# Kernel optimization log

Measured on AMD Instinct MI355X. Metric: run time of the kernel, lower is better.

Reference implementation:

```python
import jax, jax.numpy as jnp
import numpy as np


def setup_inputs() -> dict:
    key = jax.random.key(0)
    k1, k2, k3, k4 = jax.random.split(key, 4)
    B, OUT, IN, K = 64, 4096, 25088, 32
    x = jax.random.normal(k1, (B, IN), dtype=jnp.float32)
    labels = jax.random.randint(k2, (OUT, IN), 0, K, dtype=jnp.int32)
    centroids = jax.random.normal(k3, (K,), dtype=jnp.float32)
    bias = jax.random.normal(k4, (OUT,), dtype=jnp.float32)
    return {"x": x, "labels": labels, "centroids": centroids, "bias": bias}


def reference(x, labels, centroids, bias):
    # Dequantize: reconstruct weight [OUT, IN] by looking labels up in the codebook
    W = centroids[labels]                      # [OUT, IN] gather
    # addmm(bias, x, W.T): [B, IN] @ [IN, OUT] + [OUT]
    return x @ W.T + bias
```

## Files before the change

kernel.cpp:

```cpp
#include <hip/hip_runtime.h>
#include <stdint.h>

typedef float f32x4 __attribute__((ext_vector_type(4)));
typedef short bf16x8 __attribute__((ext_vector_type(8)));
typedef int   i32x4  __attribute__((ext_vector_type(4)));
typedef unsigned int u32x4 __attribute__((ext_vector_type(4)));

#define IN_DIM   25088
#define OUT_DIM  4096
#define BATCH    64
#define SPLITS   28
#define KBLK     64
#define NBLK     14
#define WG_N     128
#define LSTR     72

__device__ __forceinline__ uint32_t f2bf(float f) {
    uint32_t u = __builtin_bit_cast(uint32_t, f);
    return (u + 0x7FFFu + ((u >> 16) & 1u)) >> 16;
}
__device__ __forceinline__ uint32_t pack2(float a, float b) {
    return f2bf(a) | (f2bf(b) << 16);
}

__global__ __launch_bounds__(256) void convert_x(const float* __restrict__ x,
                                                 uint32_t* __restrict__ xb) {
    const size_t i = blockIdx.x * 256 + threadIdx.x;
    const float4 v0 = *(const float4*)(x + i * 8);
    const float4 v1 = *(const float4*)(x + i * 8 + 4);
    uint4 o;
    o.x = pack2(v0.x, v0.y); o.y = pack2(v0.z, v0.w);
    o.z = pack2(v1.x, v1.y); o.w = pack2(v1.z, v1.w);
    *(uint4*)(xb + i * 4) = o;
}

__global__ __launch_bounds__(256) void qlinear_main(
    const int*      __restrict__ labels,
    const float*    __restrict__ centroids,
    const uint16_t* __restrict__ xb,
    float*          __restrict__ part)
{
    __shared__ __align__(16) uint32_t table[1024];
    __shared__ __align__(16) uint16_t wt[WG_N * LSTR];
    __shared__ __align__(16) uint16_t xt[BATCH * LSTR];

    const int t     = threadIdx.x;
    const int wgn   = blockIdx.x & 31;
    const int split = blockIdx.x >> 5;
    const int o0    = wgn * WG_N;
    const int kbase = split * (KBLK * NBLK);

    #pragma unroll
    for (int e = 0; e < 4; ++e) {
        const int i = t + 256 * e;
        table[i] = f2bf(centroids[i & 31]) | (f2bf(centroids[i >> 5]) << 16);
    }

    const int lane = t & 63;
    const int wave = t >> 6;
    const int ln   = lane & 15;
    const int lq   = lane >> 4;

    const int srow = t >> 3;
    const int skc  = (t & 7) * 8;

    const int xrow = t >> 2;
    const int xseg = (t & 3) * 16;

    f32x4 acc[4][2] = {};

    for (int blk = 0; blk < NBLK; ++blk) {
        const int k0 = kbase + blk * KBLK;

        __syncthreads();

        #pragma unroll
        for (int p = 0; p < 4; ++p) {
            const int row = p * 32 + srow;
            const i32x4* lp = (const i32x4*)(labels + (size_t)(o0 + row) * IN_DIM + k0 + skc);
            const i32x4 l0 = __builtin_nontemporal_load(lp);
            const i32x4 l1 = __builtin_nontemporal_load(lp + 1);
            uint4 w;
            w.x = table[(uint32_t)l0.x | ((uint32_t)l0.y << 5)];
            w.y = table[(uint32_t)l0.z | ((uint32_t)l0.w << 5)];
            w.z = table[(uint32_t)l1.x | ((uint32_t)l1.y << 5)];
            w.w = table[(uint32_t)l1.z | ((uint32_t)l1.w << 5)];
            *(uint4*)(wt + row * LSTR + skc) = w;
        }
        {
            const uint16_t* xp = xb + (size_t)xrow * IN_DIM + k0 + xseg;
            const bf16x8 v0 = *(const bf16x8*)xp;
            const bf16x8 v1 = *(const bf16x8*)(xp + 8);
            *(bf16x8*)(xt + xrow * LSTR + xseg)     = v0;
            *(bf16x8*)(xt + xrow * LSTR + xseg + 8) = v1;
        }
        __syncthreads();

        #pragma unroll
        for (int ks = 0; ks < 2; ++ks) {
            const int kk = ks * 32 + lq * 8;
            bf16x8 a[4], b[2];
            #pragma unroll
            for (int mt = 0; mt < 4; ++mt)
                a[mt] = *(const bf16x8*)(xt + (mt * 16 + ln) * LSTR + kk);
            #pragma unroll
            for (int nt = 0; nt < 2; ++nt)
                b[nt] = *(const bf16x8*)(wt + (wave * 32 + nt * 16 + ln) * LSTR + kk);
            #pragma unroll
            for (int mt = 0; mt < 4; ++mt)
                #pragma unroll
                for (int nt = 0; nt < 2; ++nt)
                    acc[mt][nt] = __builtin_amdgcn_mfma_f32_16x16x32_bf16(
                        a[mt], b[nt], acc[mt][nt], 0, 0, 0);
        }
    }

    float* pout = part + (size_t)split * (BATCH * OUT_DIM);
    #pragma unroll
    for (int mt = 0; mt < 4; ++mt)
        #pragma unroll
        for (int nt = 0; nt < 2; ++nt) {
            const int o = o0 + wave * 32 + nt * 16 + ln;
            #pragma unroll
            for (int r = 0; r < 4; ++r)
                __builtin_nontemporal_store(
                    acc[mt][nt][r],
                    pout + (size_t)(mt * 16 + lq * 4 + r) * OUT_DIM + o);
        }
}

__global__ __launch_bounds__(256) void reduce_out(const float* __restrict__ part,
                                                  const float* __restrict__ bias,
                                                  float* __restrict__ out) {
    const size_t i = blockIdx.x * 256 + threadIdx.x;
    float4 s = *(const float4*)(bias + ((i * 4) & (OUT_DIM - 1)));
    #pragma unroll
    for (int sp = 0; sp < SPLITS; ++sp) {
        const f32x4 p = __builtin_nontemporal_load(
            (const f32x4*)(part + (size_t)sp * (BATCH * OUT_DIM) + i * 4));
        s.x += p.x; s.y += p.y; s.z += p.z; s.w += p.w;
    }
    *(float4*)(out + i * 4) = s;
}

extern "C" void kernel_launch(void* const* d_in, const int* in_sizes, int n_in,
                              void* d_out, int out_size, void* d_ws, size_t ws_size,
                              hipStream_t stream) {
    const float* x         = (const float*)d_in[0];
    const int*   labels    = (const int*)d_in[1];
    const float* centroids = (const float*)d_in[2];
    const float* bias      = (const float*)d_in[3];
    float* out = (float*)d_out;

    uint32_t* xb   = (uint32_t*)d_ws;
    float*    part = (float*)((char*)d_ws + (size_t)BATCH * IN_DIM * 2);

    convert_x<<<(BATCH * IN_DIM) / 2048, 256, 0, stream>>>(x, xb);
    qlinear_main<<<32 * SPLITS, 256, 0, stream>>>(labels, centroids,
                                                  (const uint16_t*)xb, part);
    reduce_out<<<(BATCH * OUT_DIM) / 1024, 256, 0, stream>>>(part, bias, out);
}
```

Measured before the change: 550.9 us.

## Prefetch label tiles into registers and replace split-K reduce with atomics

Result: no change. 545.5 us (-1.0%).

```diff
diff --git a/kernel.cpp b/kernel.cpp
--- a/kernel.cpp
+++ b/kernel.cpp
@@ -4,7 +4,6 @@
 typedef float f32x4 __attribute__((ext_vector_type(4)));
 typedef short bf16x8 __attribute__((ext_vector_type(8)));
 typedef int   i32x4  __attribute__((ext_vector_type(4)));
-typedef unsigned int u32x4 __attribute__((ext_vector_type(4)));
 
 #define IN_DIM   25088
 #define OUT_DIM  4096
@@ -15,6 +14,9 @@
 #define WG_N     128
 #define LSTR     72
 
+#define CONV_BLOCKS 784
+#define INIT_BLOCKS 64
+
 __device__ __forceinline__ uint32_t f2bf(float f) {
     uint32_t u = __builtin_bit_cast(uint32_t, f);
     return (u + 0x7FFFu + ((u >> 16) & 1u)) >> 16;
@@ -23,22 +25,35 @@
     return f2bf(a) | (f2bf(b) << 16);
 }
 
-__global__ __launch_bounds__(256) void convert_x(const float* __restrict__ x,
-                                                 uint32_t* __restrict__ xb) {
-    const size_t i = blockIdx.x * 256 + threadIdx.x;
-    const float4 v0 = *(const float4*)(x + i * 8);
-    const float4 v1 = *(const float4*)(x + i * 8 + 4);
-    uint4 o;
-    o.x = pack2(v0.x, v0.y); o.y = pack2(v0.z, v0.w);
-    o.z = pack2(v1.x, v1.y); o.w = pack2(v1.z, v1.w);
-    *(uint4*)(xb + i * 4) = o;
+__global__ __launch_bounds__(256) void prep(const float* __restrict__ x,
+                                            const float* __restrict__ bias,
+                                            uint32_t* __restrict__ xb,
+                                            float* __restrict__ out) {
+    if (blockIdx.x < CONV_BLOCKS) {
+        const size_t i = blockIdx.x * 256 + threadIdx.x;
+        const float4 v0 = *(const float4*)(x + i * 8);
+        const float4 v1 = *(const float4*)(x + i * 8 + 4);
+        uint4 o;
+        o.x = pack2(v0.x, v0.y); o.y = pack2(v0.z, v0.w);
+        o.z = pack2(v1.x, v1.y); o.w = pack2(v1.z, v1.w);
+        *(uint4*)(xb + i * 4) = o;
+    } else {
+        const size_t g = (size_t)(blockIdx.x - CONV_BLOCKS) * 256 + threadIdx.x;
+        const float4* b4 = (const float4*)bias;
+        float4* o4 = (float4*)out;
+        #pragma unroll
+        for (int r = 0; r < 4; ++r) {
+            const size_t j = g * 4 + r;
+            o4[j] = b4[j & (OUT_DIM / 4 - 1)];
+        }
+    }
 }
 
 __global__ __launch_bounds__(256) void qlinear_main(
     const int*      __restrict__ labels,
     const float*    __restrict__ centroids,
     const uint16_t* __restrict__ xb,
-    float*          __restrict__ part)
+    float*          __restrict__ out)
 {
     __shared__ __align__(16) uint32_t table[1024];
     __shared__ __align__(16) uint16_t wt[WG_N * LSTR];
@@ -67,24 +82,43 @@
     const int xrow = t >> 2;
     const int xseg = (t & 3) * 16;
 
+    const int* lbase[4];
+    #pragma unroll
+    for (int p = 0; p < 4; ++p)
+        lbase[p] = labels + (size_t)(o0 + p * 32 + srow) * IN_DIM + kbase + skc;
+
     f32x4 acc[4][2] = {};
+
+    i32x4 pl[4][2];
+    #pragma unroll
+    for (int p = 0; p < 4; ++p) {
+        pl[p][0] = __builtin_nontemporal_load((const i32x4*)lbase[p]);
+        pl[p][1] = __builtin_nontemporal_load((const i32x4*)lbase[p] + 1);
+    }
 
     for (int blk = 0; blk < NBLK; ++blk) {
         const int k0 = kbase + blk * KBLK;
+
+        i32x4 npl[4][2];
+        if (blk + 1 < NBLK) {
+            #pragma unroll
+            for (int p = 0; p < 4; ++p) {
+                const i32x4* lp = (const i32x4*)(lbase[p] + (blk + 1) * KBLK);
+                npl[p][0] = __builtin_nontemporal_load(lp);
+                npl[p][1] = __builtin_nontemporal_load(lp + 1);
+            }
+        }
 
         __syncthreads();
 
         #pragma unroll
         for (int p = 0; p < 4; ++p) {
             const int row = p * 32 + srow;
-            const i32x4* lp = (const i32x4*)(labels + (size_t)(o0 + row) * IN_DIM + k0 + skc);
-            const i32x4 l0 = __builtin_nontemporal_load(lp);
-            const i32x4 l1 = __builtin_nontemporal_load(lp + 1);
             uint4 w;
-            w.x = table[(uint32_t)l0.x | ((uint32_t)l0.y << 5)];
-            w.y = table[(uint32_t)l0.z | ((uint32_t)l0.w << 5)];
-            w.z = table[(uint32_t)l1.x | ((uint32_t)l1.y << 5)];
-            w.w = table[(uint32_t)l1.z | ((uint32_t)l1.w << 5)];
+            w.x = table[(uint32_t)pl[p][0].x | ((uint32_t)pl[p][0].y << 5)];
+            w.y = table[(uint32_t)pl[p][0].z | ((uint32_t)pl[p][0].w << 5)];
+            w.z = table[(uint32_t)pl[p][1].x | ((uint32_t)pl[p][1].y << 5)];
+            w.w = table[(uint32_t)pl[p][1].z | ((uint32_t)pl[p][1].w << 5)];
             *(uint4*)(wt + row * LSTR + skc) = w;
         }
         {
@@ -113,9 +147,14 @@
                     acc[mt][nt] = __builtin_amdgcn_mfma_f32_16x16x32_bf16(
                         a[mt], b[nt], acc[mt][nt], 0, 0, 0);
         }
+
+        #pragma unroll
+        for (int p = 0; p < 4; ++p) {
+            pl[p][0] = npl[p][0];
+            pl[p][1] = npl[p][1];
+        }
     }
 
-    float* pout = part + (size_t)split * (BATCH * OUT_DIM);
     #pragma unroll
     for (int mt = 0; mt < 4; ++mt)
         #pragma unroll
@@ -123,24 +162,9 @@
             const int o = o0 + wave * 32 + nt * 16 + ln;
             #pragma unroll
             for (int r = 0; r < 4; ++r)
-                __builtin_nontemporal_store(
-                    acc[mt][nt][r],
-                    pout + (size_t)(mt * 16 + lq * 4 + r) * OUT_DIM + o);
+                atomicAdd(out + (size_t)(mt * 16 + lq * 4 + r) * OUT_DIM + o,
+                          acc[mt][nt][r]);
         }
-}
-
-__global__ __launch_bounds__(256) void reduce_out(const float* __restrict__ part,
-                                                  const float* __restrict__ bias,
-                                                  float* __restrict__ out) {
-    const size_t i = blockIdx.x * 256 + threadIdx.x;
-    float4 s = *(const float4*)(bias + ((i * 4) & (OUT_DIM - 1)));
-    #pragma unroll
-    for (int sp = 0; sp < SPLITS; ++sp) {
-        const f32x4 p = __builtin_nontemporal_load(
-            (const f32x4*)(part + (size_t)sp * (BATCH * OUT_DIM) + i * 4));
-        s.x += p.x; s.y += p.y; s.z += p.z; s.w += p.w;
-    }
-    *(float4*)(out + i * 4) = s;
 }
 
 extern "C" void kernel_launch(void* const* d_in, const int* in_sizes, int n_in,
@@ -152,11 +176,9 @@
     const float* bias      = (const float*)d_in[3];
     float* out = (float*)d_out;
 
-    uint32_t* xb   = (uint32_t*)d_ws;
-    float*    part = (float*)((char*)d_ws + (size_t)BATCH * IN_DIM * 2);
+    uint32_t* xb = (uint32_t*)d_ws;
 
-    convert_x<<<(BATCH * IN_DIM) / 2048, 256, 0, stream>>>(x, xb);
+    prep<<<CONV_BLOCKS + INIT_BLOCKS, 256, 0, stream>>>(x, bias, xb, out);
     qlinear_main<<<32 * SPLITS, 256, 0, stream>>>(labels, centroids,
-                                                  (const uint16_t*)xb, part);
-    reduce_out<<<(BATCH * OUT_DIM) / 1024, 256, 0, stream>>>(part, bias, out);
+                                                  (const uint16_t*)xb, out);
 }
```
